# Optimization experiments

Measured on AMD Instinct MI355X. Metric: run time of the kernel, lower is better.

Reference implementation:

```python
import jax, jax.numpy as jnp
import numpy as np

N_NODES = 100000
N_EDGES = 1280000
IN_CH = 64
OUT_CH = 64


def setup_inputs() -> dict:
    key = jax.random.key(0)
    k1, k2, k3, k4 = jax.random.split(key, 4)
    x = jax.random.normal(k1, (N_NODES, IN_CH), dtype=jnp.float32)
    edge_index = jax.random.randint(k2, (2, N_EDGES), 0, N_NODES, dtype=jnp.int64)
    # GraphConv params (glorot weight, zero bias)
    scale = jnp.sqrt(6.0 / (IN_CH + OUT_CH)).astype(jnp.float32)
    W = jax.random.uniform(k3, (IN_CH, OUT_CH), dtype=jnp.float32, minval=-scale, maxval=scale)
    b = jnp.zeros((OUT_CH,), dtype=jnp.float32)
    return {"x": x, "edge_index": edge_index, "W": W, "b": b}


def reference(x, edge_index, W, b):
    # DGL GraphConv, norm='both': out = D_in^{-1/2} A^T (D_out^{-1/2} x W) + b
    src, dst = edge_index[0], edge_index[1]
    ones = jnp.ones((src.shape[0],), dtype=x.dtype)
    out_deg = jax.ops.segment_sum(ones, src, num_segments=N_NODES)
    in_deg = jax.ops.segment_sum(ones, dst, num_segments=N_NODES)
    norm_src = jnp.where(out_deg > 0, jax.lax.rsqrt(jnp.maximum(out_deg, 1.0)), 0.0)
    norm_dst = jnp.where(in_deg > 0, jax.lax.rsqrt(jnp.maximum(in_deg, 1.0)), 0.0)
    # in_feats <= out_feats: transform first, then aggregate
    h = (x * norm_src[:, None]) @ W              # [N, OUT_CH]
    msg = h[src]                                 # gather  [E, OUT_CH]
    agg = jax.ops.segment_sum(msg, dst, num_segments=N_NODES)  # scatter-add [N, OUT_CH]
    return agg * norm_dst[:, None] + b
```

## Files before the change

kernel.cpp:

```cpp
#include <hip/hip_runtime.h>
#include <hip/hip_fp16.h>

#define CH 64
#define CAP 40
#define SPILLMAX 4096
#define RANGE 12500
#define SLICES 64
#define TILE 2048
#define EPT 8
#define BSH 9
#define BKT 512

__global__ __launch_bounds__(256) void hist_kernel(const int* __restrict__ src,
                                                   unsigned short* __restrict__ partial,
                                                   int E, int N, int R)
{
    __shared__ int h[RANGE];
    int r  = blockIdx.x % R;
    int sl = blockIdx.x / R;
    int lo = r * RANGE;
    int hi = min(lo + RANGE, N);
    int span = hi - lo;
    for (int i = threadIdx.x; i < span; i += 256) h[i] = 0;
    __syncthreads();
    int per = (E + SLICES - 1) / SLICES;
    int sb = sl * per, se = min(sb + per, E);
    for (int e = sb + threadIdx.x * 4; e < se; e += 256 * 4) {
        if (e + 4 <= se) {
            int4 v = *(const int4*)(src + e);
            if (v.x >= lo && v.x < hi) atomicAdd(&h[v.x - lo], 1);
            if (v.y >= lo && v.y < hi) atomicAdd(&h[v.y - lo], 1);
            if (v.z >= lo && v.z < hi) atomicAdd(&h[v.z - lo], 1);
            if (v.w >= lo && v.w < hi) atomicAdd(&h[v.w - lo], 1);
        } else {
            for (int k = e; k < se; ++k) {
                int sv = src[k];
                if (sv >= lo && sv < hi) atomicAdd(&h[sv - lo], 1);
            }
        }
    }
    __syncthreads();
    unsigned short* pp = partial + (size_t)blockIdx.x * RANGE;
    for (int i = threadIdx.x; i < span; i += 256) pp[i] = (unsigned short)h[i];
}

__global__ __launch_bounds__(256) void odeg_reduce_kernel(const unsigned short* __restrict__ partial,
                                                          int* __restrict__ outdeg,
                                                          int N, int R)
{
    int n = blockIdx.x * 256 + threadIdx.x;
    if (n >= N) return;
    int r = n / RANGE, off = n - r * RANGE;
    int s = 0;
    #pragma unroll 8
    for (int sl = 0; sl < SLICES; ++sl)
        s += partial[(size_t)(sl * R + r) * RANGE + off];
    outdeg[n] = s;
}

__global__ __launch_bounds__(256) void prescale_kernel(const float* __restrict__ x,
                                                       const int* __restrict__ outdeg,
                                                       __half* __restrict__ xh, int N)
{
    int g = blockIdx.x * blockDim.x + threadIdx.x;
    int total = N * (CH / 8);
    if (g >= total) return;
    int node = g >> 3, sub = g & 7;
    int od = outdeg[node];
    float ns = (od > 0) ? rsqrtf((float)od) : 0.0f;
    const float4* xp = (const float4*)(x + (size_t)node * CH + sub * 8);
    float4 a = xp[0], b = xp[1];
    __half2 h0 = __floats2half2_rn(a.x * ns, a.y * ns);
    __half2 h1 = __floats2half2_rn(a.z * ns, a.w * ns);
    __half2 h2 = __floats2half2_rn(b.x * ns, b.y * ns);
    __half2 h3 = __floats2half2_rn(b.z * ns, b.w * ns);
    uint4 u;
    u.x = (unsigned)__half_as_ushort(h0.x) | ((unsigned)__half_as_ushort(h0.y) << 16);
    u.y = (unsigned)__half_as_ushort(h1.x) | ((unsigned)__half_as_ushort(h1.y) << 16);
    u.z = (unsigned)__half_as_ushort(h2.x) | ((unsigned)__half_as_ushort(h2.y) << 16);
    u.w = (unsigned)__half_as_ushort(h3.x) | ((unsigned)__half_as_ushort(h3.y) << 16);
    *(uint4*)(xh + (size_t)node * CH + sub * 8) = u;
}

__global__ __launch_bounds__(256) void binA_kernel(const int* __restrict__ dst,
                                                   int* __restrict__ tileHist,
                                                   int* __restrict__ nspill, int E)
{
    if (blockIdx.x == 0 && threadIdx.x == 0) nspill[0] = 0;
    __shared__ int h[256];
    int tid = threadIdx.x;
    int t = blockIdx.x;
    h[tid] = 0;
    __syncthreads();
    int e0 = t * TILE + tid * EPT;
    if (e0 + EPT <= E) {
        const int4* dp = (const int4*)(dst + e0);
        int4 a = dp[0], b = dp[1];
        atomicAdd(&h[a.x >> BSH], 1); atomicAdd(&h[a.y >> BSH], 1);
        atomicAdd(&h[a.z >> BSH], 1); atomicAdd(&h[a.w >> BSH], 1);
        atomicAdd(&h[b.x >> BSH], 1); atomicAdd(&h[b.y >> BSH], 1);
        atomicAdd(&h[b.z >> BSH], 1); atomicAdd(&h[b.w >> BSH], 1);
    } else {
        for (int k = e0; k < E && k < e0 + EPT; ++k) atomicAdd(&h[dst[k] >> BSH], 1);
    }
    __syncthreads();
    tileHist[t * 256 + tid] = h[tid];
}

__global__ __launch_bounds__(256) void binB_kernel(int* __restrict__ tileHist,
                                                   int* __restrict__ totals, int NT)
{
    __shared__ int sm[256];
    int b = blockIdx.x, tid = threadIdx.x;
    int C = (NT + 255) / 256;
    int vals[8];
    int s = 0;
    for (int k = 0; k < C; ++k) {
        int t = tid * C + k;
        vals[k] = (t < NT) ? tileHist[t * 256 + b] : 0;
        s += vals[k];
    }
    sm[tid] = s;
    __syncthreads();
    for (int d = 1; d < 256; d <<= 1) {
        int v = (tid >= d) ? sm[tid - d] : 0;
        __syncthreads();
        sm[tid] += v;
        __syncthreads();
    }
    int off = (tid > 0) ? sm[tid - 1] : 0;
    for (int k = 0; k < C; ++k) {
        int t = tid * C + k;
        if (t < NT) { tileHist[t * 256 + b] = off; off += vals[k]; }
    }
    if (tid == 255) totals[b] = sm[255];
}

__global__ __launch_bounds__(256) void binB2_kernel(const int* __restrict__ totals,
                                                    int* __restrict__ bucketBase, int NB)
{
    __shared__ int sm[256];
    int tid = threadIdx.x;
    sm[tid] = (tid < NB) ? totals[tid] : 0;
    __syncthreads();
    for (int d = 1; d < 256; d <<= 1) {
        int v = (tid >= d) ? sm[tid - d] : 0;
        __syncthreads();
        sm[tid] += v;
        __syncthreads();
    }
    if (tid < NB) bucketBase[tid] = (tid > 0) ? sm[tid - 1] : 0;
    if (tid == 0) bucketBase[NB] = sm[NB - 1];
}

__global__ __launch_bounds__(256) void binC_kernel(const int* __restrict__ src,
                                                   const int* __restrict__ dst,
                                                   const int* __restrict__ tileBase,
                                                   const int* __restrict__ bucketBase,
                                                   int* __restrict__ sorted, int E, int NB)
{
    __shared__ int cur[256];
    int tid = threadIdx.x;
    int t = blockIdx.x;
    cur[tid] = (tid < NB) ? bucketBase[tid] + tileBase[t * 256 + tid] : 0;
    __syncthreads();
    int e0 = t * TILE + tid * EPT;
    int s[EPT], d[EPT];
    int nk = 0;
    if (e0 + EPT <= E) {
        const int4* sp = (const int4*)(src + e0);
        const int4* dp = (const int4*)(dst + e0);
        int4 a = sp[0], b = sp[1], c = dp[0], f = dp[1];
        s[0]=a.x; s[1]=a.y; s[2]=a.z; s[3]=a.w; s[4]=b.x; s[5]=b.y; s[6]=b.z; s[7]=b.w;
        d[0]=c.x; d[1]=c.y; d[2]=c.z; d[3]=c.w; d[4]=f.x; d[5]=f.y; d[6]=f.z; d[7]=f.w;
        nk = EPT;
    } else {
        for (int k = 0; e0 + k < E && k < EPT; ++k) { s[k] = src[e0+k]; d[k] = dst[e0+k]; nk++; }
    }
    for (int k = 0; k < nk; ++k) {
        int p = d[k] >> BSH;
        int pos = atomicAdd(&cur[p], 1);
        sorted[pos] = (s[k] << BSH) | (d[k] & (BKT - 1));
    }
}

__global__ __launch_bounds__(256) void binD_kernel(const int* __restrict__ sorted,
                                                   const int* __restrict__ bucketBase,
                                                   int* __restrict__ bucket,
                                                   int* __restrict__ cnt,
                                                   int* __restrict__ spill,
                                                   int* __restrict__ nspill, int N)
{
    __shared__ int lc[BKT];
    int b = blockIdx.x, tid = threadIdx.x;
    lc[tid] = 0; lc[tid + 256] = 0;
    __syncthreads();
    int beg = bucketBase[b], end = bucketBase[b + 1];
    int nbase = b << BSH;
    for (int i = beg + tid; i < end; i += 256) {
        int v = sorted[i];
        int sv = v >> BSH;
        int dl = v & (BKT - 1);
        int pos = atomicAdd(&lc[dl], 1);
        if (pos < CAP) {
            bucket[(size_t)(nbase + dl) * CAP + pos] = sv;
        } else {
            int sp = atomicAdd(nspill, 1);
            if (sp < SPILLMAX) { spill[2*sp] = nbase + dl; spill[2*sp+1] = sv; }
        }
    }
    __syncthreads();
    int n0 = nbase + tid;
    if (n0 < N) cnt[n0] = lc[tid];
    int n1 = nbase + 256 + tid;
    if (n1 < N) cnt[n1] = lc[256 + tid];
}

__global__ __launch_bounds__(256) void agg_kernel(const __half* __restrict__ xh,
                                                  const int* __restrict__ bucket,
                                                  const int* __restrict__ cnt,
                                                  const int* __restrict__ spill,
                                                  const int* __restrict__ nspill,
                                                  __half* __restrict__ aggh, int N)
{
    int node = (blockIdx.x * blockDim.x + threadIdx.x) >> 5;
    int sl = threadIdx.x & 31;
    if (node >= N) return;
    int c = cnt[node];
    int m = (c < CAP) ? c : CAP;
    const int* bp = bucket + (size_t)node * CAP;
    float ax0 = 0, ay0 = 0, ax1 = 0, ay1 = 0, ax2 = 0, ay2 = 0, ax3 = 0, ay3 = 0;
    int j = 0;
    for (; j + 4 <= m; j += 4) {
        int s0 = bp[j + 0], s1 = bp[j + 1], s2 = bp[j + 2], s3 = bp[j + 3];
        float2 f0 = __half22float2(*(const __half2*)(xh + (size_t)s0 * CH + sl * 2));
        float2 f1 = __half22float2(*(const __half2*)(xh + (size_t)s1 * CH + sl * 2));
        float2 f2 = __half22float2(*(const __half2*)(xh + (size_t)s2 * CH + sl * 2));
        float2 f3 = __half22float2(*(const __half2*)(xh + (size_t)s3 * CH + sl * 2));
        ax0 += f0.x; ay0 += f0.y;
        ax1 += f1.x; ay1 += f1.y;
        ax2 += f2.x; ay2 += f2.y;
        ax3 += f3.x; ay3 += f3.y;
    }
    for (; j < m; ++j) {
        float2 f = __half22float2(*(const __half2*)(xh + (size_t)bp[j] * CH + sl * 2));
        ax0 += f.x; ay0 += f.y;
    }
    if (c > CAP) {
        int ns = *nspill;
        if (ns > SPILLMAX) ns = SPILLMAX;
        for (int i = 0; i < ns; ++i) {
            if (spill[2 * i] == node) {
                float2 f = __half22float2(*(const __half2*)(xh + (size_t)spill[2 * i + 1] * CH + sl * 2));
                ax0 += f.x; ay0 += f.y;
            }
        }
    }
    float nd = (c > 0) ? rsqrtf((float)c) : 0.0f;
    float rx = ((ax0 + ax1) + (ax2 + ax3)) * nd;
    float ry = ((ay0 + ay1) + (ay2 + ay3)) * nd;
    *(__half2*)(aggh + (size_t)node * CH + sl * 2) = __floats2half2_rn(rx, ry);
}

__global__ __launch_bounds__(256) void gemm_out_kernel(const __half* __restrict__ aggh,
                                                       const float* __restrict__ W,
                                                       const float* __restrict__ bias,
                                                       float* __restrict__ out, int N)
{
    int g = blockIdx.x * 256 + threadIdx.x;
    int waveId = __builtin_amdgcn_readfirstlane(g >> 6);
    int lane = threadIdx.x & 63;
    int half = waveId & 1;
    int row = ((waveId >> 1) << 6) + lane;
    if (row >= N) return;
    const int cbase = half * 32;
    float acc[32];
    #pragma unroll
    for (int i = 0; i < 32; ++i) acc[i] = 0.0f;
    const __half* xp = aggh + (size_t)row * CH;
    for (int k0 = 0; k0 < CH; k0 += 8) {
        uint4 u = *(const uint4*)(xp + k0);
        const __half2* hp = (const __half2*)&u;
        float xk[8];
        #pragma unroll
        for (int j = 0; j < 4; ++j) {
            float2 f = __half22float2(hp[j]);
            xk[2 * j] = f.x; xk[2 * j + 1] = f.y;
        }
        #pragma unroll
        for (int kk = 0; kk < 8; ++kk) {
            const float* wrow = W + (k0 + kk) * CH + cbase;
            #pragma unroll
            for (int q = 0; q < 8; ++q) {
                float4 w = *(const float4*)(wrow + q * 4);
                acc[q * 4 + 0] += xk[kk] * w.x;
                acc[q * 4 + 1] += xk[kk] * w.y;
                acc[q * 4 + 2] += xk[kk] * w.z;
                acc[q * 4 + 3] += xk[kk] * w.w;
            }
        }
    }
    float* op = out + (size_t)row * CH + cbase;
    #pragma unroll
    for (int q = 0; q < 8; ++q) {
        float4 b = *(const float4*)(bias + cbase + q * 4);
        float4 o;
        o.x = acc[q * 4 + 0] + b.x;
        o.y = acc[q * 4 + 1] + b.y;
        o.z = acc[q * 4 + 2] + b.z;
        o.w = acc[q * 4 + 3] + b.w;
        *(float4*)(op + q * 4) = o;
    }
}

extern "C" void kernel_launch(void* const* d_in, const int* in_sizes, int n_in,
                              void* d_out, int out_size, void* d_ws, size_t ws_size,
                              hipStream_t stream)
{
    const float* x    = (const float*)d_in[0];
    const int*   edge = (const int*)d_in[1];
    const float* W    = (const float*)d_in[2];
    const float* bias = (const float*)d_in[3];
    float* out = (float*)d_out;

    int N = in_sizes[0] / CH;
    int E = in_sizes[1] / 2;
    const int* src = edge;
    const int* dst = edge + E;
    int R  = (N + RANGE - 1) / RANGE;
    int NT = (E + TILE - 1) / TILE;
    int NB = (N + BKT - 1) >> BSH;

    int* nspill  = (int*)d_ws;
    int* spill   = nspill + 64;
    int* outdeg  = spill + 2 * SPILLMAX;
    int* cnt     = outdeg + N;
    int* bucket  = cnt + N;
    unsigned short* partial = (unsigned short*)(bucket + (size_t)N * CAP);
    int* tileHist   = (int*)partial;
    int* totals     = tileHist + NT * 256;
    int* bucketBase = totals + 256;
    int* sorted     = bucketBase + 320;
    size_t psz = (size_t)SLICES * R * RANGE * sizeof(unsigned short);
    size_t osz = (size_t)(NT * 256 + 256 + 320 + E) * sizeof(int);
    size_t xoff = ((((char*)partial - (char*)d_ws) + (psz > osz ? psz : osz)) + 255) & ~(size_t)255;
    __half* xh = (__half*)((char*)d_ws + xoff);
    size_t aoff = ((xoff + (size_t)N * CH * sizeof(__half)) + 255) & ~(size_t)255;
    __half* aggh = (__half*)((char*)d_ws + aoff);


    hist_kernel<<<R * SLICES, 256, 0, stream>>>(src, partial, E, N, R);
    odeg_reduce_kernel<<<(N + 255) / 256, 256, 0, stream>>>(partial, outdeg, N, R);
    prescale_kernel<<<(N * (CH / 8) + 255) / 256, 256, 0, stream>>>(x, outdeg, xh, N);
    binA_kernel<<<NT, 256, 0, stream>>>(dst, tileHist, nspill, E);
    binB_kernel<<<NB, 256, 0, stream>>>(tileHist, totals, NT);
    binB2_kernel<<<1, 256, 0, stream>>>(totals, bucketBase, NB);
    binC_kernel<<<NT, 256, 0, stream>>>(src, dst, tileHist, bucketBase, sorted, E, NB);
    binD_kernel<<<NB, 256, 0, stream>>>(sorted, bucketBase, bucket, cnt, spill, nspill, N);
    agg_kernel<<<((size_t)N * 32 + 255) / 256, 256, 0, stream>>>(xh, bucket, cnt, spill,
                                                                 nspill, aggh, N);
    int nwaves = 2 * ((N + 63) / 64);
    gemm_out_kernel<<<(nwaves + 3) / 4, 256, 0, stream>>>(aggh, W, bias, out, N);
}
```

Before: 123.5 us.

## Fuse degree reduce with prescale, inline bucket scans, widen gather loads, split GEMM

Merges the out-degree reduction and prescale kernels into one, and drops the single-block bucket-base scan kernel by recomputing the scan redundantly in each binC/binD block. The aggregation loop now reads neighbor indices with int4 vector loads and unrolls by 8. The output GEMM splits columns into quarters so each wave keeps 16 accumulators instead of 32. The aim is fewer launches and less traffic through the outdeg array, at the cost of redundant scan work per block and extra W reloads across waves.

Result: faster. 114.0 us (-7.7%).

```diff
diff --git a/kernel.cpp b/kernel.cpp
--- a/kernel.cpp
+++ b/kernel.cpp
@@ -44,42 +44,45 @@
     for (int i = threadIdx.x; i < span; i += 256) pp[i] = (unsigned short)h[i];
 }
 
-__global__ __launch_bounds__(256) void odeg_reduce_kernel(const unsigned short* __restrict__ partial,
-                                                          int* __restrict__ outdeg,
-                                                          int N, int R)
-{
-    int n = blockIdx.x * 256 + threadIdx.x;
-    if (n >= N) return;
-    int r = n / RANGE, off = n - r * RANGE;
-    int s = 0;
-    #pragma unroll 8
-    for (int sl = 0; sl < SLICES; ++sl)
-        s += partial[(size_t)(sl * R + r) * RANGE + off];
-    outdeg[n] = s;
-}
-
-__global__ __launch_bounds__(256) void prescale_kernel(const float* __restrict__ x,
-                                                       const int* __restrict__ outdeg,
-                                                       __half* __restrict__ xh, int N)
-{
-    int g = blockIdx.x * blockDim.x + threadIdx.x;
-    int total = N * (CH / 8);
-    if (g >= total) return;
-    int node = g >> 3, sub = g & 7;
-    int od = outdeg[node];
-    float ns = (od > 0) ? rsqrtf((float)od) : 0.0f;
-    const float4* xp = (const float4*)(x + (size_t)node * CH + sub * 8);
-    float4 a = xp[0], b = xp[1];
-    __half2 h0 = __floats2half2_rn(a.x * ns, a.y * ns);
-    __half2 h1 = __floats2half2_rn(a.z * ns, a.w * ns);
-    __half2 h2 = __floats2half2_rn(b.x * ns, b.y * ns);
-    __half2 h3 = __floats2half2_rn(b.z * ns, b.w * ns);
-    uint4 u;
-    u.x = (unsigned)__half_as_ushort(h0.x) | ((unsigned)__half_as_ushort(h0.y) << 16);
-    u.y = (unsigned)__half_as_ushort(h1.x) | ((unsigned)__half_as_ushort(h1.y) << 16);
-    u.z = (unsigned)__half_as_ushort(h2.x) | ((unsigned)__half_as_ushort(h2.y) << 16);
-    u.w = (unsigned)__half_as_ushort(h3.x) | ((unsigned)__half_as_ushort(h3.y) << 16);
-    *(uint4*)(xh + (size_t)node * CH + sub * 8) = u;
+__global__ __launch_bounds__(256) void rpscale_kernel(const unsigned short* __restrict__ partial,
+                                                      const float* __restrict__ x,
+                                                      __half* __restrict__ xh, int N, int R)
+{
+    __shared__ float nsl[256];
+    int tid = threadIdx.x;
+    int n0 = blockIdx.x * 256;
+    int n = n0 + tid;
+    if (n < N) {
+        int r = n / RANGE, off = n - r * RANGE;
+        int s = 0;
+        #pragma unroll 8
+        for (int sl = 0; sl < SLICES; ++sl)
+            s += partial[(size_t)(sl * R + r) * RANGE + off];
+        nsl[tid] = (s > 0) ? rsqrtf((float)s) : 0.0f;
+    } else {
+        nsl[tid] = 0.0f;
+    }
+    __syncthreads();
+    int sub = tid & 7;
+    int nl0 = tid >> 3;
+    for (int p = 0; p < 8; ++p) {
+        int nl = p * 32 + nl0;
+        int node = n0 + nl;
+        if (node >= N) break;
+        float ns = nsl[nl];
+        const float4* xp = (const float4*)(x + (size_t)node * CH + sub * 8);
+        float4 a = xp[0], b = xp[1];
+        __half2 h0 = __floats2half2_rn(a.x * ns, a.y * ns);
+        __half2 h1 = __floats2half2_rn(a.z * ns, a.w * ns);
+        __half2 h2 = __floats2half2_rn(b.x * ns, b.y * ns);
+        __half2 h3 = __floats2half2_rn(b.z * ns, b.w * ns);
+        uint4 u;
+        u.x = (unsigned)__half_as_ushort(h0.x) | ((unsigned)__half_as_ushort(h0.y) << 16);
+        u.y = (unsigned)__half_as_ushort(h1.x) | ((unsigned)__half_as_ushort(h1.y) << 16);
+        u.z = (unsigned)__half_as_ushort(h2.x) | ((unsigned)__half_as_ushort(h2.y) << 16);
+        u.w = (unsigned)__half_as_ushort(h3.x) | ((unsigned)__half_as_ushort(h3.y) << 16);
+        *(uint4*)(xh + (size_t)node * CH + sub * 8) = u;
+    }
 }
 
 __global__ __launch_bounds__(256) void binA_kernel(const int* __restrict__ dst,
@@ -136,33 +139,26 @@
     if (tid == 255) totals[b] = sm[255];
 }
 
-__global__ __launch_bounds__(256) void binB2_kernel(const int* __restrict__ totals,
-                                                    int* __restrict__ bucketBase, int NB)
-{
-    __shared__ int sm[256];
-    int tid = threadIdx.x;
-    sm[tid] = (tid < NB) ? totals[tid] : 0;
-    __syncthreads();
-    for (int d = 1; d < 256; d <<= 1) {
-        int v = (tid >= d) ? sm[tid - d] : 0;
-        __syncthreads();
-        sm[tid] += v;
-        __syncthreads();
-    }
-    if (tid < NB) bucketBase[tid] = (tid > 0) ? sm[tid - 1] : 0;
-    if (tid == 0) bucketBase[NB] = sm[NB - 1];
-}
-
 __global__ __launch_bounds__(256) void binC_kernel(const int* __restrict__ src,
                                                    const int* __restrict__ dst,
                                                    const int* __restrict__ tileBase,
-                                                   const int* __restrict__ bucketBase,
+                                                   const int* __restrict__ totals,
                                                    int* __restrict__ sorted, int E, int NB)
 {
+    __shared__ int sm[256];
     __shared__ int cur[256];
     int tid = threadIdx.x;
     int t = blockIdx.x;
-    cur[tid] = (tid < NB) ? bucketBase[tid] + tileBase[t * 256 + tid] : 0;
+    sm[tid] = (tid < NB) ? totals[tid] : 0;
+    __syncthreads();
+    for (int d = 1; d < 256; d <<= 1) {
+        int v = (tid >= d) ? sm[tid - d] : 0;
+        __syncthreads();
+        sm[tid] += v;
+        __syncthreads();
+    }
+    int bb = (tid > 0) ? sm[tid - 1] : 0;
+    cur[tid] = (tid < NB) ? bb + tileBase[t * 256 + tid] : 0;
     __syncthreads();
     int e0 = t * TILE + tid * EPT;
     int s[EPT], d[EPT];
@@ -185,17 +181,26 @@
 }
 
 __global__ __launch_bounds__(256) void binD_kernel(const int* __restrict__ sorted,
-                                                   const int* __restrict__ bucketBase,
+                                                   const int* __restrict__ totals,
                                                    int* __restrict__ bucket,
                                                    int* __restrict__ cnt,
                                                    int* __restrict__ spill,
-                                                   int* __restrict__ nspill, int N)
-{
+                                                   int* __restrict__ nspill, int N, int NB)
+{
+    __shared__ int sm[256];
     __shared__ int lc[BKT];
     int b = blockIdx.x, tid = threadIdx.x;
+    sm[tid] = (tid < NB) ? totals[tid] : 0;
     lc[tid] = 0; lc[tid + 256] = 0;
     __syncthreads();
-    int beg = bucketBase[b], end = bucketBase[b + 1];
+    for (int d = 1; d < 256; d <<= 1) {
+        int v = (tid >= d) ? sm[tid - d] : 0;
+        __syncthreads();
+        sm[tid] += v;
+        __syncthreads();
+    }
+    int beg = (b > 0) ? sm[b - 1] : 0;
+    int end = sm[b];
     int nbase = b << BSH;
     for (int i = beg + tid; i < end; i += 256) {
         int v = sorted[i];
@@ -231,12 +236,28 @@
     const int* bp = bucket + (size_t)node * CAP;
     float ax0 = 0, ay0 = 0, ax1 = 0, ay1 = 0, ax2 = 0, ay2 = 0, ax3 = 0, ay3 = 0;
     int j = 0;
+    for (; j + 8 <= m; j += 8) {
+        int4 va = *(const int4*)(bp + j);
+        int4 vb = *(const int4*)(bp + j + 4);
+        float2 f0 = __half22float2(*(const __half2*)(xh + (size_t)va.x * CH + sl * 2));
+        float2 f1 = __half22float2(*(const __half2*)(xh + (size_t)va.y * CH + sl * 2));
+        float2 f2 = __half22float2(*(const __half2*)(xh + (size_t)va.z * CH + sl * 2));
+        float2 f3 = __half22float2(*(const __half2*)(xh + (size_t)va.w * CH + sl * 2));
+        float2 f4 = __half22float2(*(const __half2*)(xh + (size_t)vb.x * CH + sl * 2));
+        float2 f5 = __half22float2(*(const __half2*)(xh + (size_t)vb.y * CH + sl * 2));
+        float2 f6 = __half22float2(*(const __half2*)(xh + (size_t)vb.z * CH + sl * 2));
+        float2 f7 = __half22float2(*(const __half2*)(xh + (size_t)vb.w * CH + sl * 2));
+        ax0 += f0.x + f4.x; ay0 += f0.y + f4.y;
+        ax1 += f1.x + f5.x; ay1 += f1.y + f5.y;
+        ax2 += f2.x + f6.x; ay2 += f2.y + f6.y;
+        ax3 += f3.x + f7.x; ay3 += f3.y + f7.y;
+    }
     for (; j + 4 <= m; j += 4) {
-        int s0 = bp[j + 0], s1 = bp[j + 1], s2 = bp[j + 2], s3 = bp[j + 3];
-        float2 f0 = __half22float2(*(const __half2*)(xh + (size_t)s0 * CH + sl * 2));
-        float2 f1 = __half22float2(*(const __half2*)(xh + (size_t)s1 * CH + sl * 2));
-        float2 f2 = __half22float2(*(const __half2*)(xh + (size_t)s2 * CH + sl * 2));
-        float2 f3 = __half22float2(*(const __half2*)(xh + (size_t)s3 * CH + sl * 2));
+        int4 va = *(const int4*)(bp + j);
+        float2 f0 = __half22float2(*(const __half2*)(xh + (size_t)va.x * CH + sl * 2));
+        float2 f1 = __half22float2(*(const __half2*)(xh + (size_t)va.y * CH + sl * 2));
+        float2 f2 = __half22float2(*(const __half2*)(xh + (size_t)va.z * CH + sl * 2));
+        float2 f3 = __half22float2(*(const __half2*)(xh + (size_t)va.w * CH + sl * 2));
         ax0 += f0.x; ay0 += f0.y;
         ax1 += f1.x; ay1 += f1.y;
         ax2 += f2.x; ay2 += f2.y;
@@ -270,13 +291,13 @@
     int g = blockIdx.x * 256 + threadIdx.x;
     int waveId = __builtin_amdgcn_readfirstlane(g >> 6);
     int lane = threadIdx.x & 63;
-    int half = waveId & 1;
-    int row = ((waveId >> 1) << 6) + lane;
+    int quarter = waveId & 3;
+    int row = ((waveId >> 2) << 6) + lane;
     if (row >= N) return;
-    const int cbase = half * 32;
-    float acc[32];
+    const int cbase = quarter * 16;
+    float acc[16];
     #pragma unroll
-    for (int i = 0; i < 32; ++i) acc[i] = 0.0f;
+    for (int i = 0; i < 16; ++i) acc[i] = 0.0f;
     const __half* xp = aggh + (size_t)row * CH;
     for (int k0 = 0; k0 < CH; k0 += 8) {
         uint4 u = *(const uint4*)(xp + k0);
@@ -291,7 +312,7 @@
         for (int kk = 0; kk < 8; ++kk) {
             const float* wrow = W + (k0 + kk) * CH + cbase;
             #pragma unroll
-            for (int q = 0; q < 8; ++q) {
+            for (int q = 0; q < 4; ++q) {
                 float4 w = *(const float4*)(wrow + q * 4);
                 acc[q * 4 + 0] += xk[kk] * w.x;
                 acc[q * 4 + 1] += xk[kk] * w.y;
@@ -302,7 +323,7 @@
     }
     float* op = out + (size_t)row * CH + cbase;
     #pragma unroll
-    for (int q = 0; q < 8; ++q) {
+    for (int q = 0; q < 4; ++q) {
         float4 b = *(const float4*)(bias + cbase + q * 4);
         float4 o;
         o.x = acc[q * 4 + 0] + b.x;
@@ -333,32 +354,27 @@
 
     int* nspill  = (int*)d_ws;
     int* spill   = nspill + 64;
-    int* outdeg  = spill + 2 * SPILLMAX;
-    int* cnt     = outdeg + N;
+    int* cnt     = spill + 2 * SPILLMAX;
     int* bucket  = cnt + N;
     unsigned short* partial = (unsigned short*)(bucket + (size_t)N * CAP);
-    int* tileHist   = (int*)partial;
-    int* totals     = tileHist + NT * 256;
-    int* bucketBase = totals + 256;
-    int* sorted     = bucketBase + 320;
+    int* tileHist = (int*)partial;
+    int* totals   = tileHist + NT * 256;
+    int* sorted   = totals + 320;
     size_t psz = (size_t)SLICES * R * RANGE * sizeof(unsigned short);
-    size_t osz = (size_t)(NT * 256 + 256 + 320 + E) * sizeof(int);
+    size_t osz = (size_t)(NT * 256 + 320 + E) * sizeof(int);
     size_t xoff = ((((char*)partial - (char*)d_ws) + (psz > osz ? psz : osz)) + 255) & ~(size_t)255;
     __half* xh = (__half*)((char*)d_ws + xoff);
     size_t aoff = ((xoff + (size_t)N * CH * sizeof(__half)) + 255) & ~(size_t)255;
     __half* aggh = (__half*)((char*)d_ws + aoff);
 
-
     hist_kernel<<<R * SLICES, 256, 0, stream>>>(src, partial, E, N, R);
-    odeg_reduce_kernel<<<(N + 255) / 256, 256, 0, stream>>>(partial, outdeg, N, R);
-    prescale_kernel<<<(N * (CH / 8) + 255) / 256, 256, 0, stream>>>(x, outdeg, xh, N);
+    rpscale_kernel<<<(N + 255) / 256, 256, 0, stream>>>(partial, x, xh, N, R);
     binA_kernel<<<NT, 256, 0, stream>>>(dst, tileHist, nspill, E);
     binB_kernel<<<NB, 256, 0, stream>>>(tileHist, totals, NT);
-    binB2_kernel<<<1, 256, 0, stream>>>(totals, bucketBase, NB);
-    binC_kernel<<<NT, 256, 0, stream>>>(src, dst, tileHist, bucketBase, sorted, E, NB);
-    binD_kernel<<<NB, 256, 0, stream>>>(sorted, bucketBase, bucket, cnt, spill, nspill, N);
+    binC_kernel<<<NT, 256, 0, stream>>>(src, dst, tileHist, totals, sorted, E, NB);
+    binD_kernel<<<NB, 256, 0, stream>>>(sorted, totals, bucket, cnt, spill, nspill, N, NB);
     agg_kernel<<<((size_t)N * 32 + 255) / 256, 256, 0, stream>>>(xh, bucket, cnt, spill,
                                                                  nspill, aggh, N);
-    int nwaves = 2 * ((N + 63) / 64);
+    int nwaves = 4 * ((N + 63) / 64);
     gemm_out_kernel<<<(nwaves + 3) / 4, 256, 0, stream>>>(aggh, W, bias, out, N);
 }
```
